# Performance work log

Measured on AMD Instinct MI355X. Metric: run time of the kernel, lower is better.

Reference implementation:

```python
import jax, jax.numpy as jnp
import numpy as np

H = 64  # GRU hidden size


def _gru_layer(x, Wih, Whh, bih, bhh):
    """PyTorch-semantics GRU layer. x: [B,T,I] -> [B,T,H].
    r = sig(Wir x + bir + Whr h + bhr); z = sig(...); n = tanh(Win x + bin + r*(Whn h + bhn))
    h' = (1-z)*n + z*h. Gate order in stacked weights: r, z, n."""
    xg = jnp.einsum('bti,gi->btg', x, Wih) + bih  # [B,T,3H], precomputed input projections

    def step(h, xg_t):
        hg = h @ Whh.T + bhh  # [B,3H]
        xr, xz, xn = jnp.split(xg_t, 3, axis=-1)
        hr, hz, hn = jnp.split(hg, 3, axis=-1)
        r = jax.nn.sigmoid(xr + hr)
        z = jax.nn.sigmoid(xz + hz)
        n = jnp.tanh(xn + r * hn)
        h_new = (1.0 - z) * n + z * h
        return h_new, h_new

    h0 = jnp.zeros((x.shape[0], H), x.dtype)
    _, ys = jax.lax.scan(step, h0, jnp.swapaxes(xg, 0, 1))  # scan over time
    return jnp.swapaxes(ys, 0, 1)  # [B,T,H]


def _gru_stack4(x, Wih0, Wih, Whh, bih, bhh):
    # layer 0 has its own input width; layers 1..3 take H->H. Inter-layer dropout
    # (p=0.2) is inference-disabled.
    y = _gru_layer(x, Wih0, Whh[0], bih[0], bhh[0])
    for l in range(3):
        y = _gru_layer(y, Wih[l], Whh[l + 1], bih[l + 1], bhh[l + 1])
    return y


def _bn_eval(x, gamma, beta, mean, var, eps=1e-5):
    return gamma * (x - mean) * jax.lax.rsqrt(var + eps) + beta


def setup_inputs() -> dict:
    key = jax.random.key(0)
    ks = jax.random.split(key, 32)
    B, T = 2048, 256
    d = {}
    d['sentiment_seq'] = jax.random.normal(ks[0], (B, T), jnp.float32)
    d['price_seq'] = jax.random.normal(ks[1], (B, T, 4), jnp.float32)
    w = lambda k, s: jax.random.normal(k, s, jnp.float32) * 0.1
    d['s_Wih0'] = w(ks[2], (192, 1)); d['s_Wih'] = w(ks[3], (3, 192, 64))
    d['s_Whh'] = w(ks[4], (4, 192, 64)); d['s_bih'] = w(ks[5], (4, 192)); d['s_bhh'] = w(ks[6], (4, 192))
    d['p_Wih0'] = w(ks[7], (192, 4)); d['p_Wih'] = w(ks[8], (3, 192, 64))
    d['p_Whh'] = w(ks[9], (4, 192, 64)); d['p_bih'] = w(ks[10], (4, 192)); d['p_bhh'] = w(ks[11], (4, 192))
    d['fc1_W'] = w(ks[12], (128, 128)); d['fc1_b'] = w(ks[13], (128,))
    d['bn1_gamma'] = jax.random.uniform(ks[14], (128,), jnp.float32, 0.5, 1.5)
    d['bn1_beta'] = w(ks[15], (128,)); d['bn1_mean'] = w(ks[16], (128,))
    d['bn1_var'] = jax.random.uniform(ks[17], (128,), jnp.float32, 0.5, 1.5)
    d['fc2_W'] = w(ks[18], (128, 128)); d['fc2_b'] = w(ks[19], (128,))
    d['bn2_gamma'] = jax.random.uniform(ks[20], (128,), jnp.float32, 0.5, 1.5)
    d['bn2_beta'] = w(ks[21], (128,)); d['bn2_mean'] = w(ks[22], (128,))
    d['bn2_var'] = jax.random.uniform(ks[23], (128,), jnp.float32, 0.5, 1.5)
    d['fc3_W'] = w(ks[24], (2, 128)); d['fc3_b'] = w(ks[25], (2,))
    return d


def reference(sentiment_seq, price_seq,
              s_Wih0, s_Wih, s_Whh, s_bih, s_bhh,
              p_Wih0, p_Wih, p_Whh, p_bih, p_bhh,
              fc1_W, fc1_b, bn1_gamma, bn1_beta, bn1_mean, bn1_var,
              fc2_W, fc2_b, bn2_gamma, bn2_beta, bn2_mean, bn2_var,
              fc3_W, fc3_b):
    # input_size[0] == 1 -> unsqueeze last dim (as in the torch module)
    s = sentiment_seq[..., None]                         # [B,T,1]
    s_out = _gru_stack4(s, s_Wih0, s_Wih, s_Whh, s_bih, s_bhh)
    p_out = _gru_stack4(price_seq, p_Wih0, p_Wih, p_Whh, p_bih, p_bhh)
    x = jnp.concatenate([s_out[:, -1, :], p_out[:, -1, :]], axis=1)  # [B,128]
    x = x @ fc1_W.T + fc1_b
    x = jax.nn.relu(_bn_eval(x, bn1_gamma, bn1_beta, bn1_mean, bn1_var))  # dropout off (eval)
    x = x @ fc2_W.T + fc2_b
    x = jax.nn.relu(_bn_eval(x, bn2_gamma, bn2_beta, bn2_mean, bn2_var))
    return x @ fc3_W.T + fc3_b  # [B,2] logits
```

## Files before the change

### kernel.cpp

```cpp
#include <hip/hip_runtime.h>

namespace {

constexpr int BB = 2048;
constexpr int TT = 256;
constexpr float L2E = 1.4426950408889634f;

typedef __attribute__((ext_vector_type(8))) short bf8;
typedef __attribute__((ext_vector_type(4))) float f4;
typedef __attribute__((ext_vector_type(2))) unsigned int u32x2;

#define MFMA16(a, b, c) __builtin_amdgcn_mfma_f32_16x16x32_bf16((a), (b), (c), 0, 0, 0)

__device__ __forceinline__ unsigned short f2bf_rne(float f) {
  unsigned int x = __float_as_uint(f);
  return (unsigned short)((x + 0x7fffu + ((x >> 16) & 1u)) >> 16);
}
__device__ __forceinline__ float sigm2(float y) {
  return __builtin_amdgcn_rcpf(1.f + __builtin_amdgcn_exp2f(-y));
}
__device__ __forceinline__ float tanh2(float y) {
  return 1.f - 2.f * __builtin_amdgcn_rcpf(__builtin_amdgcn_exp2f(y) + 1.f);
}
__device__ __forceinline__ void mk_hilo(float v, short& hi, short& lo) {
  unsigned int u = __float_as_uint(v);
  hi = (short)(u >> 16);
  float r = v - __uint_as_float(u & 0xffff0000u);
  lo = (short)(__float_as_uint(r) >> 16);
}

__device__ __forceinline__ void waitq(const unsigned* c, unsigned tgt) {
  while (__hip_atomic_load(c, __ATOMIC_ACQUIRE, __HIP_MEMORY_SCOPE_WORKGROUP) < tgt) {}
}

__global__ __launch_bounds__(1024, 4) void gru_all(
    const float* __restrict__ xs, const float* __restrict__ xp,
    const float* __restrict__ W0s, const float* __restrict__ W0p,
    const float* __restrict__ Wihs, const float* __restrict__ Wihp,
    const float* __restrict__ Whhs, const float* __restrict__ Whhp,
    const float* __restrict__ bihs, const float* __restrict__ bihp,
    const float* __restrict__ bhhs, const float* __restrict__ bhhp,
    float* __restrict__ hlast) {
  const int tid = threadIdx.x;
  const int Wv = tid >> 6, lane = tid & 63;
  const int g = Wv >> 2, w = Wv & 3;
  const int n15 = lane & 15, q = lane >> 4;
  const int blk = blockIdx.x, stack = blk >> 7;
  const int b0 = (blk & 127) * 16;

  const float* Wh = (stack ? Whhp : Whhs) + (size_t)g * 192 * 64;
  const float* bi = (stack ? bihp : bihs) + g * 192;
  const float* bh = (stack ? bhhp : bhhs) + g * 192;
  const float* Wx = (stack ? Wihp : Wihs) + (size_t)(g - 1) * 192 * 64;

  __shared__ unsigned short hb[4][4][8][16][8];
  __shared__ unsigned qdone[4];

  for (int e = tid; e < 4 * 4 * 8 * 16 * 8; e += 1024)
    ((unsigned short*)hb)[e] = 0;
  if (tid < 4) qdone[tid] = 0;
  __syncthreads();

  const int mrow = 16 * w + n15;
  const int mu = 16 * w + 4 * q;
  const int fr_w = 2 * w + (q >> 1);
  const int eo_w = (q & 1) * 4;

  const float gsc[3] = {L2E, L2E, 2.f * L2E};

  bf8 whh_[3][2];
  #pragma unroll
  for (int i = 0; i < 3; ++i) {
    #pragma unroll
    for (int kt = 0; kt < 2; ++kt) {
      const float* ph_ = Wh + (size_t)(i * 64 + mrow) * 64 + kt * 32 + q * 8;
      f4 ha = *(const f4*)ph_, hc = *(const f4*)(ph_ + 4);
      bf8 h2;
      #pragma unroll
      for (int j = 0; j < 8; ++j)
        h2[j] = (short)f2bf_rne(gsc[i] * ((j < 4) ? ha[j] : hc[j - 4]));
      whh_[i][kt] = h2;
    }
  }
  bf8 wxh_[3][2];
  if (g >= 1) {
    #pragma unroll
    for (int i = 0; i < 3; ++i) {
      #pragma unroll
      for (int kt = 0; kt < 2; ++kt) {
        const float* px_ = Wx + (size_t)(i * 64 + mrow) * 64 + kt * 32 + q * 8;
        f4 xa = *(const f4*)px_, xc = *(const f4*)(px_ + 4);
        bf8 h1;
        #pragma unroll
        for (int j = 0; j < 8; ++j)
          h1[j] = (short)f2bf_rne(gsc[i] * ((j < 4) ? xa[j] : xc[j - 4]));
        wxh_[i][kt] = h1;
      }
    }
  } else {
    const float* W0 = stack ? W0p : W0s;
    #pragma unroll
    for (int i = 0; i < 3; ++i) {
      bf8 a;
      #pragma unroll
      for (int j = 0; j < 8; ++j) a[j] = 0;
      if (q == 0) {
        if (stack) {
          #pragma unroll
          for (int d = 0; d < 4; ++d) {
            short hi, lo;
            mk_hilo(gsc[i] * W0[(size_t)(i * 64 + mrow) * 4 + d], hi, lo);
            a[d] = hi; a[4 + d] = lo;
          }
        } else {
          short hi, lo; mk_hilo(gsc[i] * W0[i * 64 + mrow], hi, lo);
          a[0] = hi; a[1] = hi; a[4] = lo; a[5] = lo;
        }
      }
      wxh_[i][0] = a; wxh_[i][1] = a;
    }
  }

  f4 bR, bZ, bNx, bNh;
  #pragma unroll
  for (int r = 0; r < 4; ++r) {
    bR[r]  = L2E * (bi[mu + r] + bh[mu + r]);
    bZ[r]  = L2E * (bi[64 + mu + r] + bh[64 + mu + r]);
    bNx[r] = 2.f * L2E * bi[128 + mu + r];
    bNh[r] = 2.f * L2E * bh[128 + mu + r];
  }
  f4 h = {0.f, 0.f, 0.f, 0.f};

  const size_t xrow = (size_t)(b0 + n15);
  float px0 = 0.f, px1 = 0.f, px2 = 0.f, px3 = 0.f;
  if (g == 0) {
    if (stack) { f4 t4 = *(const f4*)(xp + xrow * TT * 4); px0 = t4[0]; px1 = t4[1]; px2 = t4[2]; px3 = t4[3]; }
    else       { px0 = xs[xrow * TT]; }
  }

#define GRU_BODY(S)                                                            \
  {                                                                            \
    constexpr int SW = (S + 1) & 3;                                            \
    waitq(&qdone[g], 4u * (unsigned)tc);                                       \
    if (g >= 1) waitq(&qdone[g - 1], 4u * (unsigned)(tc + 1));                 \
    bf8 hh0 = *(const bf8*)&hb[g][S][q][n15][0];                               \
    bf8 hh1 = *(const bf8*)&hb[g][S][4 + q][n15][0];                           \
    bf8 xc0 = {}, xc1 = {};                                                    \
    if (g >= 1) {                                                              \
      xc0 = *(const bf8*)&hb[g - 1][SW][q][n15][0];                            \
      xc1 = *(const bf8*)&hb[g - 1][SW][4 + q][n15][0];                        \
    }                                                                          \
    f4 aR = bR, aZ = bZ, aNx = bNx, aNh = bNh;                                 \
    __builtin_amdgcn_s_setprio(1);                                             \
    aR  = MFMA16(whh_[0][0], hh0, aR);  aR  = MFMA16(whh_[0][1], hh1, aR);     \
    aZ  = MFMA16(whh_[1][0], hh0, aZ);  aZ  = MFMA16(whh_[1][1], hh1, aZ);     \
    aNh = MFMA16(whh_[2][0], hh0, aNh); aNh = MFMA16(whh_[2][1], hh1, aNh);    \
    if (g == 0) {                                                              \
      bf8 xq;                                                                  \
      _Pragma("unroll") for (int j = 0; j < 8; ++j) xq[j] = 0;                 \
      if (q == 0) {                                                            \
        if (stack) {                                                           \
          short a0 = (short)f2bf_rne(px0), a1 = (short)f2bf_rne(px1);          \
          short a2 = (short)f2bf_rne(px2), a3 = (short)f2bf_rne(px3);          \
          xq[0] = a0; xq[1] = a1; xq[2] = a2; xq[3] = a3;                      \
          xq[4] = a0; xq[5] = a1; xq[6] = a2; xq[7] = a3;                      \
        } else {                                                               \
          unsigned short xh = f2bf_rne(px0);                                   \
          float xf = __uint_as_float((unsigned)xh << 16);                      \
          unsigned short xl = f2bf_rne(px0 - xf);                              \
          xq[0] = (short)xh; xq[1] = (short)xl;                                \
          xq[4] = (short)xh; xq[5] = (short)xl;                                \
        }                                                                      \
      }                                                                        \
      aR  = MFMA16(wxh_[0][0], xq, aR);                                        \
      aZ  = MFMA16(wxh_[1][0], xq, aZ);                                        \
      aNx = MFMA16(wxh_[2][0], xq, aNx);                                       \
      if (tc + 1 < TT) {                                                       \
        if (stack) { f4 t4 = *(const f4*)(xp + (xrow * TT + tc + 1) * 4);      \
                     px0 = t4[0]; px1 = t4[1]; px2 = t4[2]; px3 = t4[3]; }     \
        else       { px0 = xs[xrow * TT + tc + 1]; }                           \
      }                                                                        \
    } else {                                                                   \
      aR  = MFMA16(wxh_[0][0], xc0, aR);  aR  = MFMA16(wxh_[0][1], xc1, aR);   \
      aZ  = MFMA16(wxh_[1][0], xc0, aZ);  aZ  = MFMA16(wxh_[1][1], xc1, aZ);   \
      aNx = MFMA16(wxh_[2][0], xc0, aNx); aNx = MFMA16(wxh_[2][1], xc1, aNx);  \
    }                                                                          \
    __builtin_amdgcn_s_setprio(0);                                             \
    _Pragma("unroll") for (int r = 0; r < 4; ++r) {                            \
      float rr = sigm2(aR[r]);                                                 \
      float zz = sigm2(aZ[r]);                                                 \
      float nn = tanh2(aNx[r] + rr * aNh[r]);                                  \
      h[r] = nn + zz * (h[r] - nn);                                            \
    }                                                                          \
    unsigned p01, p23;                                                         \
    asm("v_cvt_pk_bf16_f32 %0, %1, %2" : "=v"(p01) : "v"(h[0]), "v"(h[1]));   \
    asm("v_cvt_pk_bf16_f32 %0, %1, %2" : "=v"(p23) : "v"(h[2]), "v"(h[3]));   \
    u32x2 hiw = {p01, p23};                                                    \
    if (g < 3 && tc >= 4) waitq(&qdone[g + 1], 4u * (unsigned)(tc - 3));       \
    *(u32x2*)&hb[g][SW][fr_w][n15][eo_w] = hiw;                                \
    if (g == 3 && tc == TT - 1)                                                \
      *(f4*)&hlast[((size_t)stack * BB + b0 + n15) * 64 + mu] = h;             \
    if (lane == 0)                                                             \
      __hip_atomic_fetch_add(&qdone[g], 1u, __ATOMIC_RELEASE,                  \
                             __HIP_MEMORY_SCOPE_WORKGROUP);                    \
  }

  for (int t = 0; t < TT; t += 4) {
    { const int tc = t;     GRU_BODY(0) }
    { const int tc = t + 1; GRU_BODY(1) }
    { const int tc = t + 2; GRU_BODY(2) }
    { const int tc = t + 3; GRU_BODY(3) }
  }
#undef GRU_BODY
}

__global__ __launch_bounds__(128) void head(
    const float* __restrict__ hlast,
    const float* __restrict__ W1, const float* __restrict__ b1,
    const float* __restrict__ g1, const float* __restrict__ be1,
    const float* __restrict__ m1, const float* __restrict__ v1,
    const float* __restrict__ W2, const float* __restrict__ b2,
    const float* __restrict__ g2, const float* __restrict__ be2,
    const float* __restrict__ m2, const float* __restrict__ v2,
    const float* __restrict__ W3, const float* __restrict__ b3,
    float* __restrict__ out) {
  const int b = blockIdx.x;
  const int j = threadIdx.x;
  __shared__ float xin[128];
  __shared__ float y1[128];
  __shared__ float y2[128];
  xin[j] = (j < 64) ? hlast[(size_t)b * 64 + j]
                    : hlast[(size_t)BB * 64 + (size_t)b * 64 + (j - 64)];
  __syncthreads();
  float acc = b1[j];
  #pragma unroll 8
  for (int k = 0; k < 128; ++k) acc = fmaf(W1[j * 128 + k], xin[k], acc);
  float sc = g1[j] * rsqrtf(v1[j] + 1e-5f);
  y1[j] = fmaxf(0.f, (acc - m1[j]) * sc + be1[j]);
  __syncthreads();
  acc = b2[j];
  #pragma unroll 8
  for (int k = 0; k < 128; ++k) acc = fmaf(W2[j * 128 + k], y1[k], acc);
  sc = g2[j] * rsqrtf(v2[j] + 1e-5f);
  y2[j] = fmaxf(0.f, (acc - m2[j]) * sc + be2[j]);
  __syncthreads();
  if (j < 2) {
    float a = b3[j];
    #pragma unroll 8
    for (int k = 0; k < 128; ++k) a = fmaf(W3[j * 128 + k], y2[k], a);
    out[(size_t)b * 2 + j] = a;
  }
}

}

extern "C" void kernel_launch(void* const* d_in, const int* in_sizes, int n_in,
                              void* d_out, int out_size, void* d_ws, size_t ws_size,
                              hipStream_t stream) {
  (void)in_sizes; (void)n_in; (void)out_size; (void)ws_size;
  const float* sent   = (const float*)d_in[0];
  const float* price  = (const float*)d_in[1];
  const float* s_Wih0 = (const float*)d_in[2];
  const float* s_Wih  = (const float*)d_in[3];
  const float* s_Whh  = (const float*)d_in[4];
  const float* s_bih  = (const float*)d_in[5];
  const float* s_bhh  = (const float*)d_in[6];
  const float* p_Wih0 = (const float*)d_in[7];
  const float* p_Wih  = (const float*)d_in[8];
  const float* p_Whh  = (const float*)d_in[9];
  const float* p_bih  = (const float*)d_in[10];
  const float* p_bhh  = (const float*)d_in[11];
  const float* fc1_W  = (const float*)d_in[12];
  const float* fc1_b  = (const float*)d_in[13];
  const float* bn1_g  = (const float*)d_in[14];
  const float* bn1_b  = (const float*)d_in[15];
  const float* bn1_m  = (const float*)d_in[16];
  const float* bn1_v  = (const float*)d_in[17];
  const float* fc2_W  = (const float*)d_in[18];
  const float* fc2_b  = (const float*)d_in[19];
  const float* bn2_g  = (const float*)d_in[20];
  const float* bn2_b  = (const float*)d_in[21];
  const float* bn2_m  = (const float*)d_in[22];
  const float* bn2_v  = (const float*)d_in[23];
  const float* fc3_W  = (const float*)d_in[24];
  const float* fc3_b  = (const float*)d_in[25];
  float* out = (float*)d_out;

  float* hlast = (float*)d_ws;

  gru_all<<<dim3(256), dim3(1024), 0, stream>>>(
      sent, price, s_Wih0, p_Wih0, s_Wih, p_Wih, s_Whh, p_Whh,
      s_bih, p_bih, s_bhh, p_bhh, hlast);

  head<<<dim3(BB), dim3(128), 0, stream>>>(
      hlast, fc1_W, fc1_b, bn1_g, bn1_b, bn1_m, bn1_v,
      fc2_W, fc2_b, bn2_g, bn2_b, bn2_m, bn2_v, fc3_W, fc3_b, out);
}
```

Before: 319.6 us.

## Reorder GRU step to issue input projection before recurrent wait; share sigmoid reciprocal

```diff
diff --git a/kernel.cpp b/kernel.cpp
--- a/kernel.cpp
+++ b/kernel.cpp
@@ -15,12 +15,6 @@
 __device__ __forceinline__ unsigned short f2bf_rne(float f) {
   unsigned int x = __float_as_uint(f);
   return (unsigned short)((x + 0x7fffu + ((x >> 16) & 1u)) >> 16);
-}
-__device__ __forceinline__ float sigm2(float y) {
-  return __builtin_amdgcn_rcpf(1.f + __builtin_amdgcn_exp2f(-y));
-}
-__device__ __forceinline__ float tanh2(float y) {
-  return 1.f - 2.f * __builtin_amdgcn_rcpf(__builtin_amdgcn_exp2f(y) + 1.f);
 }
 __device__ __forceinline__ void mk_hilo(float v, short& hi, short& lo) {
   unsigned int u = __float_as_uint(v);
@@ -141,20 +135,7 @@
 #define GRU_BODY(S)                                                            \
   {                                                                            \
     constexpr int SW = (S + 1) & 3;                                            \
-    waitq(&qdone[g], 4u * (unsigned)tc);                                       \
-    if (g >= 1) waitq(&qdone[g - 1], 4u * (unsigned)(tc + 1));                 \
-    bf8 hh0 = *(const bf8*)&hb[g][S][q][n15][0];                               \
-    bf8 hh1 = *(const bf8*)&hb[g][S][4 + q][n15][0];                           \
-    bf8 xc0 = {}, xc1 = {};                                                    \
-    if (g >= 1) {                                                              \
-      xc0 = *(const bf8*)&hb[g - 1][SW][q][n15][0];                            \
-      xc1 = *(const bf8*)&hb[g - 1][SW][4 + q][n15][0];                        \
-    }                                                                          \
     f4 aR = bR, aZ = bZ, aNx = bNx, aNh = bNh;                                 \
-    __builtin_amdgcn_s_setprio(1);                                             \
-    aR  = MFMA16(whh_[0][0], hh0, aR);  aR  = MFMA16(whh_[0][1], hh1, aR);     \
-    aZ  = MFMA16(whh_[1][0], hh0, aZ);  aZ  = MFMA16(whh_[1][1], hh1, aZ);     \
-    aNh = MFMA16(whh_[2][0], hh0, aNh); aNh = MFMA16(whh_[2][1], hh1, aNh);    \
     if (g == 0) {                                                              \
       bf8 xq;                                                                  \
       _Pragma("unroll") for (int j = 0; j < 8; ++j) xq[j] = 0;                 \
@@ -172,31 +153,50 @@
           xq[4] = (short)xh; xq[5] = (short)xl;                                \
         }                                                                      \
       }                                                                        \
+      __builtin_amdgcn_s_setprio(1);                                           \
       aR  = MFMA16(wxh_[0][0], xq, aR);                                        \
       aZ  = MFMA16(wxh_[1][0], xq, aZ);                                        \
       aNx = MFMA16(wxh_[2][0], xq, aNx);                                       \
+      __builtin_amdgcn_s_setprio(0);                                           \
       if (tc + 1 < TT) {                                                       \
         if (stack) { f4 t4 = *(const f4*)(xp + (xrow * TT + tc + 1) * 4);      \
                      px0 = t4[0]; px1 = t4[1]; px2 = t4[2]; px3 = t4[3]; }     \
         else       { px0 = xs[xrow * TT + tc + 1]; }                           \
       }                                                                        \
     } else {                                                                   \
+      waitq(&qdone[g - 1], 4u * (unsigned)(tc + 1));                           \
+      bf8 xc0 = *(const bf8*)&hb[g - 1][SW][q][n15][0];                        \
+      bf8 xc1 = *(const bf8*)&hb[g - 1][SW][4 + q][n15][0];                    \
+      __builtin_amdgcn_s_setprio(1);                                           \
       aR  = MFMA16(wxh_[0][0], xc0, aR);  aR  = MFMA16(wxh_[0][1], xc1, aR);   \
       aZ  = MFMA16(wxh_[1][0], xc0, aZ);  aZ  = MFMA16(wxh_[1][1], xc1, aZ);   \
       aNx = MFMA16(wxh_[2][0], xc0, aNx); aNx = MFMA16(wxh_[2][1], xc1, aNx);  \
+      __builtin_amdgcn_s_setprio(0);                                           \
     }                                                                          \
+    waitq(&qdone[g], 4u * (unsigned)tc);                                       \
+    bf8 hh0 = *(const bf8*)&hb[g][S][q][n15][0];                               \
+    bf8 hh1 = *(const bf8*)&hb[g][S][4 + q][n15][0];                           \
+    __builtin_amdgcn_s_setprio(1);                                             \
+    aR  = MFMA16(whh_[0][0], hh0, aR);  aR  = MFMA16(whh_[0][1], hh1, aR);     \
+    aZ  = MFMA16(whh_[1][0], hh0, aZ);  aZ  = MFMA16(whh_[1][1], hh1, aZ);     \
+    aNh = MFMA16(whh_[2][0], hh0, aNh); aNh = MFMA16(whh_[2][1], hh1, aNh);    \
     __builtin_amdgcn_s_setprio(0);                                             \
+    if (g < 3 && tc >= 4) waitq(&qdone[g + 1], 4u * (unsigned)(tc - 3));       \
     _Pragma("unroll") for (int r = 0; r < 4; ++r) {                            \
-      float rr = sigm2(aR[r]);                                                 \
-      float zz = sigm2(aZ[r]);                                                 \
-      float nn = tanh2(aNx[r] + rr * aNh[r]);                                  \
+      float eR = __builtin_amdgcn_exp2f(-aR[r]);                               \
+      float eZ = __builtin_amdgcn_exp2f(-aZ[r]);                               \
+      float dR = 1.f + eR, dZ = 1.f + eZ;                                      \
+      float qq = __builtin_amdgcn_rcpf(dR * dZ);                               \
+      float rr = dZ * qq;                            \
+      float zz = dR * qq;                            \
+      float eN = __builtin_amdgcn_exp2f(aNx[r] + rr * aNh[r]);                 \
+      float nn = 1.f - 2.f * __builtin_amdgcn_rcpf(eN + 1.f);                  \
       h[r] = nn + zz * (h[r] - nn);                                            \
     }                                                                          \
     unsigned p01, p23;                                                         \
     asm("v_cvt_pk_bf16_f32 %0, %1, %2" : "=v"(p01) : "v"(h[0]), "v"(h[1]));   \
     asm("v_cvt_pk_bf16_f32 %0, %1, %2" : "=v"(p23) : "v"(h[2]), "v"(h[3]));   \
     u32x2 hiw = {p01, p23};                                                    \
-    if (g < 3 && tc >= 4) waitq(&qdone[g + 1], 4u * (unsigned)(tc - 3));       \
     *(u32x2*)&hb[g][SW][fr_w][n15][eo_w] = hiw;                                \
     if (g == 3 && tc == TT - 1)                                                \
       *(f4*)&hlast[((size_t)stack * BB + b0 + n15) * 64 + mu] = h;             \
```

Result: faster. 282.5 us (median of 2 runs) (-11.6%).
